# Optimization experiments

Measured on AMD Instinct MI355X. Metric: run time of the kernel, lower is better.

The kernel has to match this reference:

```python
import jax, jax.numpy as jnp
import numpy as np

HIDDEN = 2048
INTER = 5632
TOKENS = 8192


def setup_inputs() -> dict:
    key = jax.random.key(0)
    k1, k2, k3 = jax.random.split(key, 3)
    x = jax.random.normal(k1, (TOKENS, HIDDEN), dtype=jnp.float32)
    # gate_up_weight = [gate_weight | up_weight], shape [hidden, 2*intermediate]
    gate_up_weight = jax.random.normal(k2, (HIDDEN, 2 * INTER), dtype=jnp.float32) * (1.0 / np.sqrt(HIDDEN))
    down_weight = jax.random.normal(k3, (INTER, HIDDEN), dtype=jnp.float32) * (1.0 / np.sqrt(INTER))
    return {"x": x, "gate_up_weight": gate_up_weight, "down_weight": down_weight}


def reference(x, gate_up_weight, down_weight):
    # Fused SwiGLU expert MLP: SiLU(x @ Wg) * (x @ Wu) @ Wd
    inter = gate_up_weight.shape[1] // 2
    gate_up = jnp.matmul(x, gate_up_weight)          # [T, 2*I]
    gate, up = gate_up[:, :inter], gate_up[:, inter:]
    hidden = jax.nn.silu(gate) * up                   # [T, I]
    out = jnp.matmul(hidden, down_weight)             # [T, H]
    return out.astype(x.dtype)
```

## Files before the change

### kernel.cpp

```cpp
#include <hip/hip_runtime.h>
#include <stdint.h>

typedef unsigned short u16;
typedef __attribute__((ext_vector_type(8))) __bf16 bf16x8;
typedef __attribute__((ext_vector_type(8))) u16 u16x8;
typedef __attribute__((ext_vector_type(4))) float f32x4;

#define HID 2048
#define INTER 5632
#define TOKENS 8192

__device__ __forceinline__ u16 f2bf(float f) {
  uint32_t u = __builtin_bit_cast(uint32_t, f);
  u += 0x7fffu + ((u >> 16) & 1u);
  return (u16)(u >> 16);
}

__device__ __forceinline__ void gld_lds16(const u16* g, u16* l) {
  __builtin_amdgcn_global_load_lds(
      (const __attribute__((address_space(1))) unsigned int*)g,
      (__attribute__((address_space(3))) unsigned int*)l, 16, 0, 0);
}


__global__ void k_cvt_x(const float* __restrict__ in, u16* __restrict__ out) {
  size_t i = (size_t)blockIdx.x * 256 + threadIdx.x;
  const float4* p = (const float4*)(in + i * 8);
  float4 a = p[0], b = p[1];
  u16x8 o;
  o[0] = f2bf(a.x); o[1] = f2bf(a.y); o[2] = f2bf(a.z); o[3] = f2bf(a.w);
  o[4] = f2bf(b.x); o[5] = f2bf(b.y); o[6] = f2bf(b.z); o[7] = f2bf(b.w);
  *(u16x8*)(out + i * 8) = o;
}

__global__ void k_transpose(const float* __restrict__ in, u16* __restrict__ out,
                            int R, int C) {
  __shared__ float t[32][33];
  int c0 = blockIdx.x * 32, r0 = blockIdx.y * 32;
  int tx = threadIdx.x, ty = threadIdx.y;
#pragma unroll
  for (int r = 0; r < 4; ++r) {
    int i = ty + r * 8;
    t[i][tx] = in[(size_t)(r0 + i) * C + c0 + tx];
  }
  __syncthreads();
#pragma unroll
  for (int r = 0; r < 4; ++r) {
    int i = ty + r * 8;
    out[(size_t)(c0 + i) * R + r0 + tx] = f2bf(t[tx][i]);
  }
}

__global__ __launch_bounds__(256, 2) void k_gemm1(
    const u16* __restrict__ xb, const u16* __restrict__ w1t,
    u16* __restrict__ hid) {
  __shared__ __align__(16) u16 sA[128 * 64];
  __shared__ __align__(16) u16 sG[64 * 64];
  __shared__ __align__(16) u16 sU[64 * 64];
  const int K = HID;
  int brow = blockIdx.y * 128, bcol = blockIdx.x * 64;
  int tid = threadIdx.x, lane = tid & 63, wid = tid >> 6;
  int wm = wid >> 1, wn = wid & 1;
  f32x4 accg[4][2] = {}, accu[4][2] = {};
  const u16* gA = xb + (size_t)brow * K;
  const u16* gG = w1t + (size_t)bcol * K;
  const u16* gU = w1t + (size_t)(bcol + INTER) * K;
  int tr = tid >> 3;
  int tc = (tid & 7) * 8;
  int cb = lane & 15, kb = (lane >> 4) * 8;

  for (int kt = 0; kt < K / 64; ++kt) {
    int k0 = kt * 64;
#pragma unroll
    for (int r = 0; r < 4; ++r) {
      int row = r * 32 + tr;
      gld_lds16(gA + (size_t)row * K + k0 + tc, &sA[row * 64 + tc]);
    }
#pragma unroll
    for (int r = 0; r < 2; ++r) {
      int row = r * 32 + tr;
      gld_lds16(gG + (size_t)row * K + k0 + tc, &sG[row * 64 + tc]);
      gld_lds16(gU + (size_t)row * K + k0 + tc, &sU[row * 64 + tc]);
    }
    __syncthreads();
#pragma unroll
    for (int ks = 0; ks < 2; ++ks) {
      int kk = ks * 32 + kb;
      bf16x8 af[4];
#pragma unroll
      for (int m = 0; m < 4; ++m)
        af[m] = *(const bf16x8*)&sA[(wm * 64 + m * 16 + cb) * 64 + kk];
#pragma unroll
      for (int n = 0; n < 2; ++n) {
        bf16x8 bg = *(const bf16x8*)&sG[(wn * 32 + n * 16 + cb) * 64 + kk];
        bf16x8 bu = *(const bf16x8*)&sU[(wn * 32 + n * 16 + cb) * 64 + kk];
#pragma unroll
        for (int m = 0; m < 4; ++m) {
          accg[m][n] = __builtin_amdgcn_mfma_f32_16x16x32_bf16(af[m], bg, accg[m][n], 0, 0, 0);
          accu[m][n] = __builtin_amdgcn_mfma_f32_16x16x32_bf16(af[m], bu, accu[m][n], 0, 0, 0);
        }
      }
    }
    __syncthreads();
  }
  int rb = (lane >> 4) * 4;
#pragma unroll
  for (int m = 0; m < 4; ++m)
#pragma unroll
    for (int n = 0; n < 2; ++n) {
      int col = bcol + wn * 32 + n * 16 + cb;
#pragma unroll
      for (int i = 0; i < 4; ++i) {
        int row = brow + wm * 64 + m * 16 + rb + i;
        float g = accg[m][n][i], u = accu[m][n][i];
        float h = g / (1.0f + __expf(-g)) * u;
        hid[(size_t)row * INTER + col] = f2bf(h);
      }
    }
}

__global__ __launch_bounds__(256, 2) void k_gemm2(
    const u16* __restrict__ hid, const u16* __restrict__ w2t,
    float* __restrict__ out) {
  __shared__ __align__(16) u16 sA[128 * 64];
  __shared__ __align__(16) u16 sB[128 * 64];
  const int K = INTER;
  int brow = blockIdx.y * 128, bcol = blockIdx.x * 128;
  int tid = threadIdx.x, lane = tid & 63, wid = tid >> 6;
  int wm = wid >> 1, wn = wid & 1;
  f32x4 acc[4][4] = {};
  const u16* gA = hid + (size_t)brow * K;
  const u16* gB = w2t + (size_t)bcol * K;
  int tr = tid >> 3, tc = (tid & 7) * 8;
  int cb = lane & 15, kb = (lane >> 4) * 8;

  for (int kt = 0; kt < K / 64; ++kt) {
    int k0 = kt * 64;
#pragma unroll
    for (int r = 0; r < 4; ++r) {
      int row = r * 32 + tr;
      gld_lds16(gA + (size_t)row * K + k0 + tc, &sA[row * 64 + tc]);
      gld_lds16(gB + (size_t)row * K + k0 + tc, &sB[row * 64 + tc]);
    }
    __syncthreads();
#pragma unroll
    for (int ks = 0; ks < 2; ++ks) {
      int kk = ks * 32 + kb;
      bf16x8 af[4], bq[4];
#pragma unroll
      for (int m = 0; m < 4; ++m)
        af[m] = *(const bf16x8*)&sA[(wm * 64 + m * 16 + cb) * 64 + kk];
#pragma unroll
      for (int n = 0; n < 4; ++n)
        bq[n] = *(const bf16x8*)&sB[(wn * 64 + n * 16 + cb) * 64 + kk];
#pragma unroll
      for (int n = 0; n < 4; ++n)
#pragma unroll
        for (int m = 0; m < 4; ++m)
          acc[m][n] = __builtin_amdgcn_mfma_f32_16x16x32_bf16(af[m], bq[n], acc[m][n], 0, 0, 0);
    }
    __syncthreads();
  }
  int rb = (lane >> 4) * 4;
#pragma unroll
  for (int m = 0; m < 4; ++m)
#pragma unroll
    for (int n = 0; n < 4; ++n) {
      int col = bcol + wn * 64 + n * 16 + cb;
#pragma unroll
      for (int i = 0; i < 4; ++i) {
        int row = brow + wm * 64 + m * 16 + rb + i;
        out[(size_t)row * HID + col] = acc[m][n][i];
      }
    }
}


extern "C" void kernel_launch(void* const* d_in, const int* in_sizes, int n_in,
                              void* d_out, int out_size, void* d_ws, size_t ws_size,
                              hipStream_t stream) {
  const float* x  = (const float*)d_in[0];
  const float* w1 = (const float*)d_in[1];
  const float* w2 = (const float*)d_in[2];
  float* out = (float*)d_out;

  const size_t off_xb  = 0;
  const size_t off_w1t = 33554432;
  const size_t off_w2t = off_w1t + 46137344;
  const size_t off_hid = off_w2t + 23068672;
  const size_t need    = off_hid + 92274688;
  if (ws_size < need) return;

  char* ws = (char*)d_ws;
  u16* xb  = (u16*)(ws + off_xb);
  u16* w1t = (u16*)(ws + off_w1t);
  u16* w2t = (u16*)(ws + off_w2t);
  u16* hid = (u16*)(ws + off_hid);

  k_cvt_x<<<TOKENS * HID / 8 / 256, 256, 0, stream>>>(x, xb);
  dim3 tb(32, 8);
  k_transpose<<<dim3((2 * INTER) / 32, HID / 32), tb, 0, stream>>>(w1, w1t, HID, 2 * INTER);
  k_transpose<<<dim3(HID / 32, INTER / 32), tb, 0, stream>>>(w2, w2t, INTER, HID);

  k_gemm1<<<dim3(INTER / 64, TOKENS / 128), 256, 0, stream>>>(xb, w1t, hid);
  k_gemm2<<<dim3(HID / 128, TOKENS / 128), 256, 0, stream>>>(hid, w2t, out);
}
```

Measured before the change: 804.9 us.

## Rewrite both GEMMs as 256x256 double-buffered 8-phase MFMA pipelines

Both GEMM kernels become 512-thread blocks computing 256x256 tiles. LDS is double-buffered with XOR-swizzled chunk layout, and each k-tile is split into four load/compute phases separated by barriers, explicit vmcnt waits and setprio. Block indices are remapped so neighbouring blocks share operand tiles in cache. The aim is to overlap global-to-LDS loads with MFMA work, cut LDS bank conflicts and raise per-block data reuse. The cost is higher register and LDS pressure (128 KB of shared memory per block) and fragile hand-tuned wait counts.

```diff
diff --git a/kernel.cpp b/kernel.cpp
--- a/kernel.cpp
+++ b/kernel.cpp
@@ -51,126 +51,186 @@
   }
 }
 
-__global__ __launch_bounds__(256, 2) void k_gemm1(
+
+#define STAGE(dst, srcBase, stride, kt)                                        \
+  do {                                                                         \
+    const int _k0 = (kt) * 64;                                                 \
+    _Pragma("unroll") for (int _r = 0; _r < 2; ++_r) {                         \
+      const int _prow = _r * 64 + wid * 8 + srow;                              \
+      const u16* _src = (srcBase) + (size_t)_prow * (stride) + _k0 +           \
+                        ((schunk ^ (_prow & 7)) * 8);                          \
+      gld_lds16(_src, (dst) + _prow * 64 + schunk * 8);                        \
+    }                                                                          \
+  } while (0)
+
+#define LOAD_A(bufp, mh)                                                       \
+  do {                                                                         \
+    _Pragma("unroll") for (int _jj = 0; _jj < 4; ++_jj) {                      \
+      const int _row = ((mh)*4 + _jj) * 32 + wm * 16 + cb;                     \
+      _Pragma("unroll") for (int _ks = 0; _ks < 2; ++_ks) {                    \
+        const int _ch = (_ks * 4 + hi) ^ (cb & 7);                             \
+        aF[_jj][_ks] = *(const bf16x8*)((bufp) + _row * 64 + _ch * 8);         \
+      }                                                                        \
+    }                                                                          \
+  } while (0)
+
+#define LOAD_B(bufp, nh)                                                       \
+  do {                                                                         \
+    _Pragma("unroll") for (int _nn = 0; _nn < 2; ++_nn) {                      \
+      const int _row = ((nh)*2 + _nn) * 64 + wn * 16 + cb;                     \
+      _Pragma("unroll") for (int _ks = 0; _ks < 2; ++_ks) {                    \
+        const int _ch = (_ks * 4 + hi) ^ (cb & 7);                             \
+        bF[_nn][_ks] = *(const bf16x8*)((bufp) + _row * 64 + _ch * 8);         \
+      }                                                                        \
+    }                                                                          \
+  } while (0)
+
+#define MMA_Q(mh, nh)                                                          \
+  do {                                                                         \
+    _Pragma("unroll") for (int _ks = 0; _ks < 2; ++_ks)                        \
+    _Pragma("unroll") for (int _jj = 0; _jj < 4; ++_jj)                        \
+    _Pragma("unroll") for (int _nn = 0; _nn < 2; ++_nn)                        \
+      acc[(mh)*4 + _jj][(nh)*2 + _nn] =                                        \
+          __builtin_amdgcn_mfma_f32_16x16x32_bf16(                             \
+              aF[_jj][_ks], bF[_nn][_ks], acc[(mh)*4 + _jj][(nh)*2 + _nn],     \
+              0, 0, 0);                                                        \
+  } while (0)
+
+#define KTILE_BODY(bufA, bufB, nA, nB, gA0, gB0, gA1, gB1, STRIDE, hn, tn)     \
+  do {                                                                         \
+                                                            \
+    if (hn) STAGE(nA, gA0, STRIDE, tn);                                        \
+    LOAD_A(bufA, 0); LOAD_B(bufB, 0);                                          \
+    __builtin_amdgcn_s_barrier();                                              \
+    __builtin_amdgcn_s_setprio(1); MMA_Q(0, 0); __builtin_amdgcn_s_setprio(0); \
+    __builtin_amdgcn_s_barrier();                                              \
+                                                            \
+    if (hn) STAGE(nB, gB0, STRIDE, tn);                                        \
+    LOAD_A(bufA, 1);                                                           \
+    __builtin_amdgcn_s_barrier();                                              \
+    __builtin_amdgcn_s_setprio(1); MMA_Q(1, 0); __builtin_amdgcn_s_setprio(0); \
+    __builtin_amdgcn_sched_barrier(0);                                         \
+    if (hn) asm volatile("s_waitcnt vmcnt(4)" ::: "memory");                   \
+    else    asm volatile("s_waitcnt vmcnt(0)" ::: "memory");                   \
+    __builtin_amdgcn_s_barrier();                                              \
+                                                            \
+    if (hn) STAGE((nA) + 128 * 64, gA1, STRIDE, tn);                           \
+    LOAD_B(bufB, 1);                                                           \
+    __builtin_amdgcn_s_barrier();                                              \
+    __builtin_amdgcn_s_setprio(1); MMA_Q(1, 1); __builtin_amdgcn_s_setprio(0); \
+    __builtin_amdgcn_s_barrier();                                              \
+                                                            \
+    if (hn) STAGE((nB) + 128 * 64, gB1, STRIDE, tn);                           \
+    LOAD_A(bufA, 0);                                                           \
+    __builtin_amdgcn_s_barrier();                                              \
+    __builtin_amdgcn_s_setprio(1); MMA_Q(0, 1); __builtin_amdgcn_s_setprio(0); \
+    __builtin_amdgcn_sched_barrier(0);                                         \
+    if (hn) asm volatile("s_waitcnt vmcnt(2)" ::: "memory");                   \
+    __builtin_amdgcn_s_barrier();                                              \
+  } while (0)
+
+__global__ __launch_bounds__(512, 2) void k_gemm1_8ph(
     const u16* __restrict__ xb, const u16* __restrict__ w1t,
     u16* __restrict__ hid) {
-  __shared__ __align__(16) u16 sA[128 * 64];
-  __shared__ __align__(16) u16 sG[64 * 64];
-  __shared__ __align__(16) u16 sU[64 * 64];
-  const int K = HID;
-  int brow = blockIdx.y * 128, bcol = blockIdx.x * 64;
-  int tid = threadIdx.x, lane = tid & 63, wid = tid >> 6;
-  int wm = wid >> 1, wn = wid & 1;
-  f32x4 accg[4][2] = {}, accu[4][2] = {};
-  const u16* gA = xb + (size_t)brow * K;
-  const u16* gG = w1t + (size_t)bcol * K;
-  const u16* gU = w1t + (size_t)(bcol + INTER) * K;
-  int tr = tid >> 3;
-  int tc = (tid & 7) * 8;
-  int cb = lane & 15, kb = (lane >> 4) * 8;
-
-  for (int kt = 0; kt < K / 64; ++kt) {
-    int k0 = kt * 64;
-#pragma unroll
-    for (int r = 0; r < 4; ++r) {
-      int row = r * 32 + tr;
-      gld_lds16(gA + (size_t)row * K + k0 + tc, &sA[row * 64 + tc]);
-    }
-#pragma unroll
-    for (int r = 0; r < 2; ++r) {
-      int row = r * 32 + tr;
-      gld_lds16(gG + (size_t)row * K + k0 + tc, &sG[row * 64 + tc]);
-      gld_lds16(gU + (size_t)row * K + k0 + tc, &sU[row * 64 + tc]);
-    }
-    __syncthreads();
-#pragma unroll
-    for (int ks = 0; ks < 2; ++ks) {
-      int kk = ks * 32 + kb;
-      bf16x8 af[4];
-#pragma unroll
-      for (int m = 0; m < 4; ++m)
-        af[m] = *(const bf16x8*)&sA[(wm * 64 + m * 16 + cb) * 64 + kk];
-#pragma unroll
-      for (int n = 0; n < 2; ++n) {
-        bf16x8 bg = *(const bf16x8*)&sG[(wn * 32 + n * 16 + cb) * 64 + kk];
-        bf16x8 bu = *(const bf16x8*)&sU[(wn * 32 + n * 16 + cb) * 64 + kk];
-#pragma unroll
-        for (int m = 0; m < 4; ++m) {
-          accg[m][n] = __builtin_amdgcn_mfma_f32_16x16x32_bf16(af[m], bg, accg[m][n], 0, 0, 0);
-          accu[m][n] = __builtin_amdgcn_mfma_f32_16x16x32_bf16(af[m], bu, accu[m][n], 0, 0, 0);
-        }
-      }
-    }
-    __syncthreads();
-  }
-  int rb = (lane >> 4) * 4;
-#pragma unroll
-  for (int m = 0; m < 4; ++m)
-#pragma unroll
-    for (int n = 0; n < 2; ++n) {
-      int col = bcol + wn * 32 + n * 16 + cb;
+  __shared__ __align__(16) u16 sA[2][256 * 64];
+  __shared__ __align__(16) u16 sB[2][256 * 64];
+  const int NT = HID / 64;
+  const int o = blockIdx.x;
+  const int swz = (o & 7) * 176 + (o >> 3);
+  const int brow = (swz / 44) * 256, bcol = (swz % 44) * 128;
+
+  const int tid = threadIdx.x, lane = tid & 63, wid = tid >> 6;
+  const int wm = wid >> 2, wn = wid & 3;
+  const int cb = lane & 15, hi = lane >> 4;
+  const int srow = lane >> 3, schunk = lane & 7;
+
+  f32x4 acc[8][4] = {};
+  bf16x8 aF[4][2], bF[2][2];
+
+  const u16* gA0 = xb + (size_t)brow * HID;
+  const u16* gA1 = gA0 + (size_t)128 * HID;
+  const u16* gB0 = w1t + (size_t)bcol * HID;
+  const u16* gB1 = w1t + (size_t)(INTER + bcol) * HID;
+
+  STAGE(sA[0], gA0, HID, 0);
+  STAGE(sB[0], gB0, HID, 0);
+  STAGE(sA[0] + 128 * 64, gA1, HID, 0);
+  STAGE(sB[0] + 128 * 64, gB1, HID, 0);
+  asm volatile("s_waitcnt vmcnt(2)" ::: "memory");
+  __builtin_amdgcn_s_barrier();
+
+  for (int t = 0; t < NT; ++t) {
+    u16* bufA = sA[t & 1];
+    u16* bufB = sB[t & 1];
+    u16* nA = sA[(t & 1) ^ 1];
+    u16* nB = sB[(t & 1) ^ 1];
+    const bool hn = (t + 1 < NT);
+    KTILE_BODY(bufA, bufB, nA, nB, gA0, gB0, gA1, gB1, HID, hn, t + 1);
+  }
+
+#pragma unroll
+  for (int j = 0; j < 8; ++j)
+#pragma unroll
+    for (int nn = 0; nn < 2; ++nn) {
+      const int col = bcol + nn * 64 + wn * 16 + cb;
 #pragma unroll
       for (int i = 0; i < 4; ++i) {
-        int row = brow + wm * 64 + m * 16 + rb + i;
-        float g = accg[m][n][i], u = accu[m][n][i];
+        const int row = brow + j * 32 + wm * 16 + hi * 4 + i;
+        float g = acc[j][nn][i], u = acc[j][nn + 2][i];
         float h = g / (1.0f + __expf(-g)) * u;
         hid[(size_t)row * INTER + col] = f2bf(h);
       }
     }
 }
 
-__global__ __launch_bounds__(256, 2) void k_gemm2(
+__global__ __launch_bounds__(512, 2) void k_gemm2_8ph(
     const u16* __restrict__ hid, const u16* __restrict__ w2t,
     float* __restrict__ out) {
-  __shared__ __align__(16) u16 sA[128 * 64];
-  __shared__ __align__(16) u16 sB[128 * 64];
-  const int K = INTER;
-  int brow = blockIdx.y * 128, bcol = blockIdx.x * 128;
-  int tid = threadIdx.x, lane = tid & 63, wid = tid >> 6;
-  int wm = wid >> 1, wn = wid & 1;
-  f32x4 acc[4][4] = {};
-  const u16* gA = hid + (size_t)brow * K;
-  const u16* gB = w2t + (size_t)bcol * K;
-  int tr = tid >> 3, tc = (tid & 7) * 8;
-  int cb = lane & 15, kb = (lane >> 4) * 8;
-
-  for (int kt = 0; kt < K / 64; ++kt) {
-    int k0 = kt * 64;
-#pragma unroll
-    for (int r = 0; r < 4; ++r) {
-      int row = r * 32 + tr;
-      gld_lds16(gA + (size_t)row * K + k0 + tc, &sA[row * 64 + tc]);
-      gld_lds16(gB + (size_t)row * K + k0 + tc, &sB[row * 64 + tc]);
-    }
-    __syncthreads();
-#pragma unroll
-    for (int ks = 0; ks < 2; ++ks) {
-      int kk = ks * 32 + kb;
-      bf16x8 af[4], bq[4];
-#pragma unroll
-      for (int m = 0; m < 4; ++m)
-        af[m] = *(const bf16x8*)&sA[(wm * 64 + m * 16 + cb) * 64 + kk];
-#pragma unroll
-      for (int n = 0; n < 4; ++n)
-        bq[n] = *(const bf16x8*)&sB[(wn * 64 + n * 16 + cb) * 64 + kk];
-#pragma unroll
-      for (int n = 0; n < 4; ++n)
-#pragma unroll
-        for (int m = 0; m < 4; ++m)
-          acc[m][n] = __builtin_amdgcn_mfma_f32_16x16x32_bf16(af[m], bq[n], acc[m][n], 0, 0, 0);
-    }
-    __syncthreads();
-  }
-  int rb = (lane >> 4) * 4;
-#pragma unroll
-  for (int m = 0; m < 4; ++m)
+  __shared__ __align__(16) u16 sA[2][256 * 64];
+  __shared__ __align__(16) u16 sB[2][256 * 64];
+  const int NT = INTER / 64;
+  const int o = blockIdx.x;
+  const int swz = (o & 7) * 32 + (o >> 3);
+  const int brow = (swz / 8) * 256, bcol = (swz % 8) * 256;
+
+  const int tid = threadIdx.x, lane = tid & 63, wid = tid >> 6;
+  const int wm = wid >> 2, wn = wid & 3;
+  const int cb = lane & 15, hi = lane >> 4;
+  const int srow = lane >> 3, schunk = lane & 7;
+
+  f32x4 acc[8][4] = {};
+  bf16x8 aF[4][2], bF[2][2];
+
+  const u16* gA0 = hid + (size_t)brow * INTER;
+  const u16* gA1 = gA0 + (size_t)128 * INTER;
+  const u16* gB0 = w2t + (size_t)bcol * INTER;
+  const u16* gB1 = w2t + (size_t)(bcol + 128) * INTER;
+
+  STAGE(sA[0], gA0, INTER, 0);
+  STAGE(sB[0], gB0, INTER, 0);
+  STAGE(sA[0] + 128 * 64, gA1, INTER, 0);
+  STAGE(sB[0] + 128 * 64, gB1, INTER, 0);
+  asm volatile("s_waitcnt vmcnt(2)" ::: "memory");
+  __builtin_amdgcn_s_barrier();
+
+  for (int t = 0; t < NT; ++t) {
+    u16* bufA = sA[t & 1];
+    u16* bufB = sB[t & 1];
+    u16* nA = sA[(t & 1) ^ 1];
+    u16* nB = sB[(t & 1) ^ 1];
+    const bool hn = (t + 1 < NT);
+    KTILE_BODY(bufA, bufB, nA, nB, gA0, gB0, gA1, gB1, INTER, hn, t + 1);
+  }
+
+#pragma unroll
+  for (int j = 0; j < 8; ++j)
 #pragma unroll
     for (int n = 0; n < 4; ++n) {
-      int col = bcol + wn * 64 + n * 16 + cb;
+      const int col = bcol + n * 64 + wn * 16 + cb;
 #pragma unroll
       for (int i = 0; i < 4; ++i) {
-        int row = brow + wm * 64 + m * 16 + rb + i;
-        out[(size_t)row * HID + col] = acc[m][n][i];
+        const int row = brow + j * 32 + wm * 16 + hi * 4 + i;
+        out[(size_t)row * HID + col] = acc[j][n][i];
       }
     }
 }
@@ -202,6 +262,6 @@
   k_transpose<<<dim3((2 * INTER) / 32, HID / 32), tb, 0, stream>>>(w1, w1t, HID, 2 * INTER);
   k_transpose<<<dim3(HID / 32, INTER / 32), tb, 0, stream>>>(w2, w2t, INTER, HID);
 
-  k_gemm1<<<dim3(INTER / 64, TOKENS / 128), 256, 0, stream>>>(xb, w1t, hid);
-  k_gemm2<<<dim3(HID / 128, TOKENS / 128), 256, 0, stream>>>(hid, w2t, out);
-}
+  k_gemm1_8ph<<<(TOKENS / 256) * (INTER / 128), 512, 0, stream>>>(xb, w1t, hid);
+  k_gemm2_8ph<<<(TOKENS / 256) * (HID / 256), 512, 0, stream>>>(hid, w2t, out);
+}
```

Result: slower. 1.001 ms (+24.3%).
